# Optimization experiments

Measured on AMD Instinct MI355X. Metric: run time of the kernel, lower is better.

Reference implementation:

```python
import jax, jax.numpy as jnp
import numpy as np

G, N, F, D, L, H, MAXN, K = 256, 128, 128, 256, 4, 8, 512, 5
T = G * N
S = K + 1  # subgraph seq len: self + top-5 context nodes


def _ln(x, g, b, eps=1e-5):
    m = x.mean(-1, keepdims=True)
    v = ((x - m) ** 2).mean(-1, keepdims=True)
    return (x - m) / jnp.sqrt(v + eps) * g + b


def setup_inputs() -> dict:
    key = jax.random.key(0)
    ks = iter(jax.random.split(key, 40))
    r = lambda shape, s=0.02: jax.random.normal(next(ks), shape, jnp.float32) * s
    return {
        "x": jax.random.normal(next(ks), (T, F), jnp.float32),
        "W_raw": r((F, D)), "b_raw": jnp.zeros((D,), jnp.float32),
        "wl_emb": r((100, D)), "pos_emb": r((MAXN, D)), "hop_emb": r((MAXN, D)),
        "ln_g": jnp.ones((D,), jnp.float32), "ln_b": jnp.zeros((D,), jnp.float32),
        "Wqkv": r((L, D, 3 * D)), "bqkv": jnp.zeros((L, 3 * D), jnp.float32),
        "Wo": r((L, D, D)), "bo": jnp.zeros((L, D), jnp.float32),
        "n1_g": jnp.ones((L, D), jnp.float32), "n1_b": jnp.zeros((L, D), jnp.float32),
        "W1": r((L, D, 4 * D)), "b1": jnp.zeros((L, 4 * D), jnp.float32),
        "W2": r((L, 4 * D, D)), "b2": jnp.zeros((L, D), jnp.float32),
        "n2_g": jnp.ones((L, D), jnp.float32), "n2_b": jnp.zeros((L, D), jnp.float32),
        "W_res": r((F, D)), "b_res": jnp.zeros((D,), jnp.float32),
        "edge_index": jax.random.randint(next(ks), (2, 4 * T), 0, T, jnp.int32),
        "batch": jnp.repeat(jnp.arange(G, dtype=jnp.int32), N),
        "num_graphs": G,
    }


def _forward(x, W_raw, b_raw, wl_emb, pos_emb, hop_emb, ln_g, ln_b,
             Wqkv, bqkv, Wo, bo, n1_g, n1_b, W1, b1, W2, b2, n2_g, n2_b,
             W_res, b_res):
    # Inference path (training=False): intimacy matrix = eye(N) per graph, wl_codes = 0.
    eye = jnp.eye(N, dtype=x.dtype)
    _, topi = jax.lax.top_k(eye, K)                       # [N,K]: self first, then smallest tied-zero idxs
    idx = jnp.concatenate([jnp.arange(N)[:, None], topi], axis=1)  # [N,S] subgraph node ids (local)
    xg = x.reshape(G, N, F)
    sub_x = xg[:, idx]                                    # [G,N,S,F] gather per-node subgraphs
    raw = sub_x @ W_raw + b_raw                           # [G,N,S,D]
    dist = eye[jnp.arange(N)[:, None], idx]               # [N,S] intimacy of center to subgraph nodes
    hop_ids = jnp.where(dist > 0, (5.0 / jnp.maximum(dist, 1e-30)).astype(jnp.int32), MAXN - 1)
    hop_ids = jnp.clip(hop_ids, 0, MAXN - 1)              # [N,S]
    emb = raw + pos_emb[:S] + wl_emb[0] + hop_emb[hop_ids]
    h = _ln(emb, ln_g, ln_b).reshape(T, S, D)             # dropout is identity in eval
    # residual_mapped: only first num_graphs rows get non-zero residual (as in the source)
    res = jnp.zeros((T, S, D), x.dtype)
    res = res.at[:G].set((x @ W_res + b_res).reshape(G, N, D)[:, :S])
    hd = D // H
    scale = 1.0 / jnp.sqrt(jnp.asarray(hd, x.dtype))
    for l in range(L):
        qkv = h @ Wqkv[l] + bqkv[l]                       # [T,S,3D]
        q, k, v = jnp.split(qkv, 3, axis=-1)
        q = q.reshape(T, S, H, hd)
        k = k.reshape(T, S, H, hd)
        v = v.reshape(T, S, H, hd)
        sc = jnp.einsum('bqhd,bkhd->bhqk', q, k) * scale  # [T,H,S,S]
        a = jax.nn.softmax(sc, axis=-1)
        o = jnp.einsum('bhqk,bkhd->bqhd', a, v).reshape(T, S, D)
        attn = o @ Wo[l] + bo[l]
        h = _ln(h + attn + res, n1_g[l], n1_b[l])
        ff = jax.nn.gelu(h @ W1[l] + b1[l], approximate=False) @ W2[l] + b2[l]
        h = _ln(h + ff + res, n2_g[l], n2_b[l])
    return h[:, 0]                                        # [T,D] CLS/center-node output


def reference(x, W_raw, b_raw, wl_emb, pos_emb, hop_emb, ln_g, ln_b,
              Wqkv, bqkv, Wo, bo, n1_g, n1_b, W1, b1, W2, b2, n2_g, n2_b,
              W_res, b_res, edge_index, batch, num_graphs):
    # edge_index / batch / num_graphs are unused numerics in the eval path
    # (equal-size graphs assumed: batch = repeat(arange(G), N)).
    return _forward(x, W_raw, b_raw, wl_emb, pos_emb, hop_emb, ln_g, ln_b,
                    Wqkv, bqkv, Wo, bo, n1_g, n1_b, W1, b1, W2, b2, n2_g, n2_b,
                    W_res, b_res)
```

## Files before the change

### kernel.cpp

```cpp
#include <hip/hip_runtime.h>
#include <hip/hip_bf16.h>


#define TB 4
#define NROW 24

typedef float f32x4 __attribute__((ext_vector_type(4)));
typedef short bfv8  __attribute__((ext_vector_type(8)));

__device__ __forceinline__ float bf2f(__hip_bfloat16 v) { return __bfloat162float(v); }
__device__ __forceinline__ __hip_bfloat16 f2bf(float v) { return __float2bfloat16(v); }
__device__ __forceinline__ float bfs2f(short s) { return __uint_as_float(((unsigned)(unsigned short)s) << 16); }
__device__ __forceinline__ int swz(int row, int cb) { return row*512 + (cb ^ ((row & 7) << 4)); }
__device__ __forceinline__ float gelu_f(float v) { return 0.5f*v*(1.f + erff(v*0.70710678118654752f)); }
__device__ __forceinline__ float unpk(unsigned p, int hi) {
  return __uint_as_float(hi ? (p & 0xffff0000u) : (p << 16));
}

#define OWQ 0u
#define OWO 786432u
#define OW1 1048576u
#define OW2 2097152u
#define WS_ELEMS 3145728u
#define RESOFF    6291456u
#define ACTOFF    7864320u

__global__ __launch_bounds__(256) void gb_prep_kernel(
    const float* __restrict__ Wqkv, const float* __restrict__ Wo,
    const float* __restrict__ W1,   const float* __restrict__ W2,
    __hip_bfloat16* __restrict__ ws)
{
  int fg   = blockIdx.x * 4 + (threadIdx.x >> 6);
  int lane = threadIdx.x & 63;
  int layer = fg / 1536, r = fg % 1536;
  const float* src; int K, N, fl; unsigned dstbase;
  if (r < 384)       { src = Wqkv + layer*196608; K = 256;  N = 768;  fl = r;       dstbase = OWQ + layer*196608u; }
  else if (r < 512)  { src = Wo   + layer*65536;  K = 256;  N = 256;  fl = r - 384; dstbase = OWO + layer*65536u;  }
  else if (r < 1024) { src = W1   + layer*262144; K = 256;  N = 1024; fl = r - 512; dstbase = OW1 + layer*262144u; }
  else               { src = W2   + layer*262144; K = 1024; N = 256;  fl = r - 1024;dstbase = OW2 + layer*262144u; }
  int nk = K >> 5;
  int nt = fl / nk, ks = fl % nk;
  int n  = nt*16 + (lane & 15);
  int k0 = ks*32 + (lane >> 4)*8;
  __align__(16) __hip_bfloat16 tmp[8];
  #pragma unroll
  for (int j = 0; j < 8; ++j) tmp[j] = f2bf(src[(size_t)(k0 + j)*N + n]);
  *(uint4*)(ws + dstbase + (unsigned)fl*512u + lane*8) = *(const uint4*)tmp;
}

template<int NKTOT, class LoadA>
__device__ __forceinline__ void gemm_ks(const __hip_bfloat16* __restrict__ p,
                                        LoadA loadA, f32x4 (&C)[4][2])
{
  const unsigned ST = 4u*(unsigned)NKTOT*512u;
  bfv8 B[3][4];
  bfv8 a[2][4];
  #pragma unroll
  for (int i = 0; i < 4; ++i) {
    C[i][0] = (f32x4){0.f,0.f,0.f,0.f};
    C[i][1] = (f32x4){0.f,0.f,0.f,0.f};
  }
  #pragma unroll
  for (int k = 0; k < 4; ++k) B[0][k] = *(const bfv8*)(p + k*512);
  {
    const __hip_bfloat16* q = p + ST;
    #pragma unroll
    for (int k = 0; k < 4; ++k) B[1][k] = *(const bfv8*)(q + k*512);
  }
  loadA(0, a);
  #pragma unroll
  for (int s = 0; s < 8; ++s) {
    if (s + 2 < 8) {
      const __hip_bfloat16* q = p + (unsigned)((s+2) & 3)*ST + (unsigned)((s+2) >> 2)*2048u;
      #pragma unroll
      for (int k = 0; k < 4; ++k) B[(s+2)%3][k] = *(const bfv8*)(q + k*512);
    }
    if (s == 4) loadA(1, a);
    #pragma unroll
    for (int k = 0; k < 4; ++k) {
      C[s&3][0] = __builtin_amdgcn_mfma_f32_16x16x32_bf16(a[0][k], B[s%3][k], C[s&3][0], 0,0,0);
      C[s&3][1] = __builtin_amdgcn_mfma_f32_16x16x32_bf16(a[1][k], B[s%3][k], C[s&3][1], 0,0,0);
    }
  }
}

template<int NKTOT, class LoadA>
__device__ __forceinline__ void gemm_ksq(const __hip_bfloat16* __restrict__ p,
                                         LoadA loadA, f32x4 (&C)[2][2])
{
  const unsigned ST = 8u*(unsigned)NKTOT*512u;
  bfv8 a[2][2];
  #pragma unroll
  for (int i = 0; i < 2; ++i) {
    C[i][0] = (f32x4){0.f,0.f,0.f,0.f};
    C[i][1] = (f32x4){0.f,0.f,0.f,0.f};
  }
  #pragma unroll
  for (int q = 0; q < 4; ++q) {
    loadA(q, a);
    #pragma unroll
    for (int i = 0; i < 2; ++i) {
      const __hip_bfloat16* b = p + (unsigned)i*ST + (unsigned)q*1024u;
      bfv8 B0 = *(const bfv8*)(b);
      bfv8 B1 = *(const bfv8*)(b + 512);
      C[i][0] = __builtin_amdgcn_mfma_f32_16x16x32_bf16(a[0][0], B0, C[i][0], 0,0,0);
      C[i][1] = __builtin_amdgcn_mfma_f32_16x16x32_bf16(a[1][0], B0, C[i][1], 0,0,0);
      C[i][0] = __builtin_amdgcn_mfma_f32_16x16x32_bf16(a[0][1], B1, C[i][0], 0,0,0);
      C[i][1] = __builtin_amdgcn_mfma_f32_16x16x32_bf16(a[1][1], B1, C[i][1], 0,0,0);
    }
  }
}

template<int NKTOT, class LoadA>
__device__ __forceinline__ void gemm_ksq_acc(const __hip_bfloat16* __restrict__ p,
                                             LoadA loadA, f32x4 (&C)[2][2])
{
  const unsigned ST = 8u*(unsigned)NKTOT*512u;
  bfv8 a[2][2];
  #pragma unroll
  for (int q = 0; q < 4; ++q) {
    loadA(q, a);
    #pragma unroll
    for (int i = 0; i < 2; ++i) {
      const __hip_bfloat16* b = p + (unsigned)i*ST + (unsigned)q*1024u;
      bfv8 B0 = *(const bfv8*)(b);
      bfv8 B1 = *(const bfv8*)(b + 512);
      C[i][0] = __builtin_amdgcn_mfma_f32_16x16x32_bf16(a[0][0], B0, C[i][0], 0,0,0);
      C[i][1] = __builtin_amdgcn_mfma_f32_16x16x32_bf16(a[1][0], B0, C[i][1], 0,0,0);
      C[i][0] = __builtin_amdgcn_mfma_f32_16x16x32_bf16(a[0][1], B1, C[i][0], 0,0,0);
      C[i][1] = __builtin_amdgcn_mfma_f32_16x16x32_bf16(a[1][1], B1, C[i][1], 0,0,0);
    }
  }
}

__device__ __forceinline__ void ln24_norm(float* z, float* redbuf, float g, float b, int tid) {
  const int lane = tid & 63, wid = tid >> 6;
  float s1[NROW], s2[NROW];
  #pragma unroll
  for (int r = 0; r < NROW; ++r) { float v = z[r]; s1[r] = v; s2[r] = v*v; }
  #pragma unroll
  for (int off = 32; off; off >>= 1) {
    #pragma unroll
    for (int r = 0; r < NROW; ++r) {
      s1[r] += __shfl_down(s1[r], off, 64);
      s2[r] += __shfl_down(s2[r], off, 64);
    }
  }
  if (lane == 0) {
    #pragma unroll
    for (int r = 0; r < NROW; ++r) { redbuf[wid*48 + r] = s1[r]; redbuf[wid*48 + 24 + r] = s2[r]; }
  }
  __syncthreads();
  #pragma unroll
  for (int r = 0; r < NROW; ++r) {
    float S1 = redbuf[r] + redbuf[48+r] + redbuf[96+r] + redbuf[144+r];
    float S2 = redbuf[24+r] + redbuf[72+r] + redbuf[120+r] + redbuf[168+r];
    float m  = S1 * (1.0f/256.0f);
    float var = S2 * (1.0f/256.0f) - m*m;
    float iv = rsqrtf(var + 1e-5f);
    z[r] = (z[r] - m) * iv * g + b;
  }
  __syncthreads();
}


__global__ __launch_bounds__(256) void mk_embed(
    const float* __restrict__ x,
    const float* __restrict__ W_raw, const float* __restrict__ b_raw,
    const float* __restrict__ wl_emb, const float* __restrict__ pos_emb,
    const float* __restrict__ hop_emb,
    const float* __restrict__ ln_g, const float* __restrict__ ln_b,
    const float* __restrict__ W_res, const float* __restrict__ b_res,
    __hip_bfloat16* __restrict__ h0, float* __restrict__ res, int t0)
{
  __shared__ float xbuf[24][128];
  __shared__ float zb[24][256];
  __shared__ float part[2][24][8];
  __shared__ float stat[24][2];
  const int tid = threadIdx.x;
  const int bt  = blockIdx.x;

  for (int idx = tid; idx < 24*128; idx += 256) {
    int tt = idx / 768, rem = idx % 768;
    int s = rem >> 7, f = rem & 127;
    int t = t0 + bt*4 + tt, g = t >> 7, i = t & 127;
    int node;
    if (s < 2) node = i;
    else { int j = s - 2; node = (j < i) ? j : (j + 1); }
    xbuf[tt*6+s][f] = x[(g*128 + node)*128 + f];
  }
  __syncthreads();

  {
    float z[NROW];
    #pragma unroll
    for (int r = 0; r < NROW; ++r) z[r] = 0.f;
    #pragma unroll 2
    for (int f4 = 0; f4 < 32; ++f4) {
      float w0 = W_raw[(f4*4+0)*256 + tid];
      float w1 = W_raw[(f4*4+1)*256 + tid];
      float w2 = W_raw[(f4*4+2)*256 + tid];
      float w3 = W_raw[(f4*4+3)*256 + tid];
      #pragma unroll
      for (int r = 0; r < NROW; ++r) {
        float4 xv = *(const float4*)(&xbuf[r][f4*4]);
        z[r] += xv.x*w0 + xv.y*w1 + xv.z*w2 + xv.w*w3;
      }
    }
    float br  = b_raw[tid];
    float wl  = wl_emb[tid];
    float hp0 = hop_emb[5*256 + tid];
    float hp1 = hop_emb[511*256 + tid];
    float p[6];
    #pragma unroll
    for (int s = 0; s < 6; ++s) p[s] = pos_emb[s*256 + tid];
    #pragma unroll
    for (int r = 0; r < NROW; ++r) {
      int s = r % 6;
      zb[r][tid] = z[r] + br + p[s] + wl + ((s < 2) ? hp0 : hp1);
    }
  }
  __syncthreads();

  if (tid < 192) {
    int row = tid >> 3, seg = tid & 7;
    float s1 = 0.f, s2 = 0.f;
    #pragma unroll
    for (int i = 0; i < 32; ++i) {
      int col = seg*32 + ((i + tid) & 31);
      float v = zb[row][col];
      s1 += v; s2 += v*v;
    }
    part[0][row][seg] = s1; part[1][row][seg] = s2;
  }
  __syncthreads();
  if (tid < 24) {
    float S1 = 0.f, S2 = 0.f;
    #pragma unroll
    for (int k = 0; k < 8; ++k) { S1 += part[0][tid][k]; S2 += part[1][tid][k]; }
    float m = S1 * (1.0f/256.0f);
    float var = S2 * (1.0f/256.0f) - m*m;
    stat[tid][0] = m; stat[tid][1] = rsqrtf(var + 1e-5f);
  }
  __syncthreads();
  {
    float g = ln_g[tid], b = ln_b[tid];
    #pragma unroll
    for (int r = 0; r < NROW; ++r) {
      float v = (zb[r][tid] - stat[r][0]) * stat[r][1] * g + b;
      h0[(size_t)(bt*24 + r)*256 + tid] = f2bf(v);
    }
  }

  if (t0 + bt*4 < 256) {
    __syncthreads();
    for (int idx = tid; idx < 24*128; idx += 256) {
      int tt = idx / 768, rem = idx % 768;
      int s = rem >> 7, f = rem & 127;
      int t = t0 + bt*4 + tt;
      xbuf[tt*6+s][f] = x[(t*128 + s)*128 + f];
    }
    __syncthreads();
    float resv[NROW];
    float brr = b_res[tid];
    #pragma unroll
    for (int r = 0; r < NROW; ++r) resv[r] = brr;
    #pragma unroll 2
    for (int f4 = 0; f4 < 32; ++f4) {
      float w0 = W_res[(f4*4+0)*256 + tid];
      float w1 = W_res[(f4*4+1)*256 + tid];
      float w2 = W_res[(f4*4+2)*256 + tid];
      float w3 = W_res[(f4*4+3)*256 + tid];
      #pragma unroll
      for (int r = 0; r < NROW; ++r) {
        float4 xv = *(const float4*)(&xbuf[r][f4*4]);
        resv[r] += xv.x*w0 + xv.y*w1 + xv.z*w2 + xv.w*w3;
      }
    }
    #pragma unroll
    for (int r = 0; r < NROW; ++r)
      res[(size_t)((t0 + bt*4)*6 + r)*256 + tid] = resv[r];
  }
}

__device__ __forceinline__ void stageA(const __hip_bfloat16* __restrict__ src,
                                       int row0, int stride, char* aT, int tid) {
  #pragma unroll
  for (int k = 0; k < 4; ++k) {
    int cid = tid + k*256;
    int row = cid >> 5, cc = cid & 31;
    uint4 v = *(const uint4*)(src + (size_t)(row0 + row)*stride + cc*8);
    *(uint4*)(aT + swz(row, cc*16)) = v;
  }
}
__device__ __forceinline__ void stageA512(const __hip_bfloat16* __restrict__ src,
                                          int row0, int stride, char* aT, int tid) {
  #pragma unroll
  for (int k = 0; k < 2; ++k) {
    int cid = tid + k*512;
    int row = cid >> 5, cc = cid & 31;
    uint4 v = *(const uint4*)(src + (size_t)(row0 + row)*stride + cc*8);
    *(uint4*)(aT + swz(row, cc*16)) = v;
  }
}

__global__ __launch_bounds__(256) void mk_qkv(
    const __hip_bfloat16* __restrict__ h, const __hip_bfloat16* __restrict__ Wf,
    const float* __restrict__ bqkv_l, __hip_bfloat16* __restrict__ qkv)
{
  __shared__ __align__(16) char aT[16384];
  const int tid = threadIdx.x;
  const int lane = tid & 63, wid = tid >> 6;
  const int l15 = lane & 15, l4 = lane >> 4;
  const int row0 = blockIdx.x * 32;

  stageA(h, row0, 256, aT, tid);
  __syncthreads();

  auto lA = [&](int kh, bfv8 (&a)[2][4]) {
    #pragma unroll
    for (int k = 0; k < 4; ++k) {
      a[0][k] = *(const bfv8*)(aT + swz(l15,      (kh*4 + k)*64 + l4*16));
      a[1][k] = *(const bfv8*)(aT + swz(16 + l15, (kh*4 + k)*64 + l4*16));
    }
  };

  #pragma unroll 1
  for (int sub = 0; sub < 3; ++sub) {
    f32x4 C[4][2];
    gemm_ks<8>(Wf + (unsigned)(sub*16 + wid)*8u*512u + lane*8, lA, C);
    #pragma unroll
    for (int i = 0; i < 4; ++i) {
      int col = sub*256 + (wid + i*4)*16 + l15;
      float bb = bqkv_l[col];
      #pragma unroll
      for (int j = 0; j < 4; ++j) {
        qkv[(size_t)(row0 + l4*4 + j)*768 + col]      = f2bf(C[i][0][j] + bb);
        qkv[(size_t)(row0 + 16 + l4*4 + j)*768 + col] = f2bf(C[i][1][j] + bb);
      }
    }
  }
}

__global__ __launch_bounds__(256) void mk_attn(__hip_bfloat16* __restrict__ qkv)
{
  const int tid = threadIdx.x;
  const int tl = tid >> 3, hh = tid & 7;
  const size_t rowbase = (size_t)(blockIdx.x*32 + tl)*6;
  const int cb = hh*32;

  #pragma unroll 1
  for (int q = 0; q < 6; ++q) {
    const __hip_bfloat16* qr = qkv + (rowbase + q)*768 + cb;
    bfv8 qv[4];
    #pragma unroll
    for (int p4 = 0; p4 < 4; ++p4) qv[p4] = *(const bfv8*)(qr + p4*8);
    float a[6]; float mx = -1e30f;
    #pragma unroll
    for (int sp = 0; sp < 6; ++sp) {
      const __hip_bfloat16* kr = qkv + (rowbase + sp)*768 + 256 + cb;
      float s = 0.f;
      #pragma unroll
      for (int p4 = 0; p4 < 4; ++p4) {
        bfv8 kv = *(const bfv8*)(kr + p4*8);
        #pragma unroll
        for (int j = 0; j < 8; ++j) s += bfs2f(qv[p4][j]) * bfs2f(kv[j]);
      }
      a[sp] = s * 0.17677669529663687f;
      mx = fmaxf(mx, a[sp]);
    }
    float sum = 0.f;
    #pragma unroll
    for (int sp = 0; sp < 6; ++sp) { a[sp] = __expf(a[sp] - mx); sum += a[sp]; }
    float inv = 1.f / sum;
    #pragma unroll
    for (int sp = 0; sp < 6; ++sp) a[sp] *= inv;
    float oc[32];
    #pragma unroll
    for (int j = 0; j < 32; ++j) oc[j] = 0.f;
    #pragma unroll
    for (int sp = 0; sp < 6; ++sp) {
      const __hip_bfloat16* vr = qkv + (rowbase + sp)*768 + 512 + cb;
      float asp = a[sp];
      #pragma unroll
      for (int p4 = 0; p4 < 4; ++p4) {
        bfv8 vv = *(const bfv8*)(vr + p4*8);
        #pragma unroll
        for (int j = 0; j < 8; ++j) oc[p4*8 + j] += asp * bfs2f(vv[j]);
      }
    }
    __hip_bfloat16* orow = qkv + (rowbase + q)*768 + cb;
    #pragma unroll
    for (int p4 = 0; p4 < 4; ++p4) {
      __align__(16) __hip_bfloat16 ob[8];
      #pragma unroll
      for (int j = 0; j < 8; ++j) ob[j] = f2bf(oc[p4*8 + j]);
      *(uint4*)(orow + p4*8) = *(const uint4*)ob;
    }
  }
}

__global__ __launch_bounds__(512) void mk_wo_ln(
    const __hip_bfloat16* __restrict__ qkv ,
    const __hip_bfloat16* __restrict__ h,
    const float* __restrict__ res,
    const __hip_bfloat16* __restrict__ Wf, const float* __restrict__ bo_l,
    const float* __restrict__ gln, const float* __restrict__ bln,
    __hip_bfloat16* __restrict__ h1, int t0)
{
  __shared__ __align__(16) char smem[37120];
  char* aT = smem;
  float (*zb)[256]      = (float (*)[256])smem;
  float (*part)[32][16] = (float (*)[32][16])(smem + 32768);
  float (*stat)[2]      = (float (*)[2])(smem + 32768 + 4096);
  const int tid = threadIdx.x;
  const int lane = tid & 63, wid = tid >> 6;
  const int l15 = lane & 15, l4 = lane >> 4;
  const int row0 = blockIdx.x * 32;

  stageA512(qkv, row0, 768, aT, tid);
  __syncthreads();

  auto lAq = [&](int q, bfv8 (&a)[2][2]) {
    #pragma unroll
    for (int k = 0; k < 2; ++k) {
      a[0][k] = *(const bfv8*)(aT + swz(l15,      (q*2 + k)*64 + l4*16));
      a[1][k] = *(const bfv8*)(aT + swz(16 + l15, (q*2 + k)*64 + l4*16));
    }
  };

  {
    f32x4 C[2][2];
    gemm_ksq<8>(Wf + (unsigned)wid*8u*512u + lane*8, lAq, C);
    __syncthreads();
    #pragma unroll
    for (int i = 0; i < 2; ++i) {
      int col = (wid + i*8)*16 + l15;
      #pragma unroll
      for (int j = 0; j < 4; ++j) {
        zb[l4*4 + j][col]      = C[i][0][j];
        zb[16 + l4*4 + j][col] = C[i][1][j];
      }
    }
  }
  __syncthreads();

  #pragma unroll 4
  for (int it = 0; it < 16; ++it) {
    int idx = tid + it*512, row = idx >> 8, col = idx & 255;
    float v = zb[row][col] + bf2f(h[(size_t)(row0 + row)*256 + col]) + bo_l[col];
    int grow = t0*6 + row0 + row;
    if (grow < 1536) v += res[(size_t)grow*256 + col];
    zb[row][col] = v;
  }
  __syncthreads();

  {
    int row = tid >> 4, seg = tid & 15;
    float s1 = 0.f, s2 = 0.f;
    #pragma unroll
    for (int i = 0; i < 16; ++i) {
      int col = seg*16 + ((i + tid) & 15);
      float v = zb[row][col];
      s1 += v; s2 += v*v;
    }
    part[0][row][seg] = s1; part[1][row][seg] = s2;
  }
  __syncthreads();
  if (tid < 32) {
    float S1 = 0.f, S2 = 0.f;
    #pragma unroll
    for (int k = 0; k < 16; ++k) { S1 += part[0][tid][k]; S2 += part[1][tid][k]; }
    float m = S1 * (1.0f/256.0f);
    float var = S2 * (1.0f/256.0f) - m*m;
    stat[tid][0] = m; stat[tid][1] = rsqrtf(var + 1e-5f);
  }
  __syncthreads();
  #pragma unroll 4
  for (int it = 0; it < 16; ++it) {
    int idx = tid + it*512, row = idx >> 8, col = idx & 255;
    float v = (zb[row][col] - stat[row][0]) * stat[row][1] * gln[col] + bln[col];
    h1[(size_t)(row0 + row)*256 + col] = f2bf(v);
  }
}

__global__ __launch_bounds__(512) void mk_ffn(
    const __hip_bfloat16* __restrict__ h1,
    const __hip_bfloat16* __restrict__ W1f, const __hip_bfloat16* __restrict__ W2f,
    const float* __restrict__ b1_l, const float* __restrict__ b2_l,
    const float* __restrict__ gln, const float* __restrict__ bln,
    const float* __restrict__ res, __hip_bfloat16* __restrict__ hout,
    float* __restrict__ outp, int t0)
{
  __shared__ __align__(16) char smem[37120];
  char* aT = smem;
  char* gT = smem + 16384;
  float (*zf)[256]      = (float (*)[256])smem;
  float (*part)[32][16] = (float (*)[32][16])(smem + 32768);
  float (*stat)[2]      = (float (*)[2])(smem + 32768 + 4096);
  const int tid = threadIdx.x;
  const int lane = tid & 63, wid = tid >> 6;
  const int l15 = lane & 15, l4 = lane >> 4;
  const int row0 = blockIdx.x * 32;

  stageA512(h1, row0, 256, aT, tid);
  __syncthreads();

  auto lAq = [&](int q, bfv8 (&a)[2][2]) {
    #pragma unroll
    for (int k = 0; k < 2; ++k) {
      a[0][k] = *(const bfv8*)(aT + swz(l15,      (q*2 + k)*64 + l4*16));
      a[1][k] = *(const bfv8*)(aT + swz(16 + l15, (q*2 + k)*64 + l4*16));
    }
  };
  auto lGq = [&](int q, bfv8 (&a)[2][2]) {
    #pragma unroll
    for (int k = 0; k < 2; ++k) {
      a[0][k] = *(const bfv8*)(gT + swz(l15,      (q*2 + k)*64 + l4*16));
      a[1][k] = *(const bfv8*)(gT + swz(16 + l15, (q*2 + k)*64 + l4*16));
    }
  };

  f32x4 Cff[2][2];
  #pragma unroll
  for (int i = 0; i < 2; ++i) {
    Cff[i][0] = (f32x4){0.f,0.f,0.f,0.f};
    Cff[i][1] = (f32x4){0.f,0.f,0.f,0.f};
  }

  #pragma unroll 1
  for (int ch = 0; ch < 4; ++ch) {
    {
      f32x4 C[2][2];
      gemm_ksq<8>(W1f + (unsigned)(ch*16 + wid)*8u*512u + lane*8, lAq, C);
      #pragma unroll
      for (int i = 0; i < 2; ++i) {
        int colR = (wid + i*8)*16 + l15;
        float bb = b1_l[ch*256 + colR];
        int col2 = colR*2;
        #pragma unroll
        for (int j = 0; j < 4; ++j) {
          *(__hip_bfloat16*)(gT + swz(l4*4 + j, col2))      = f2bf(gelu_f(C[i][0][j] + bb));
          *(__hip_bfloat16*)(gT + swz(16 + l4*4 + j, col2)) = f2bf(gelu_f(C[i][1][j] + bb));
        }
      }
    }
    __syncthreads();
    gemm_ksq_acc<32>(W2f + (unsigned)(wid*32 + ch*8)*512u + lane*8, lGq, Cff);
    __syncthreads();
  }

  #pragma unroll
  for (int i = 0; i < 2; ++i) {
    int col = (wid + i*8)*16 + l15;
    float b2v = b2_l[col];
    #pragma unroll
    for (int j = 0; j < 4; ++j) {
      int r0 = l4*4 + j, r1 = 16 + l4*4 + j;
      float v0 = Cff[i][0][j] + bf2f(h1[(size_t)(row0 + r0)*256 + col]) + b2v;
      float v1 = Cff[i][1][j] + bf2f(h1[(size_t)(row0 + r1)*256 + col]) + b2v;
      int g0 = t0*6 + row0 + r0, g1 = t0*6 + row0 + r1;
      if (g0 < 1536) v0 += res[(size_t)g0*256 + col];
      if (g1 < 1536) v1 += res[(size_t)g1*256 + col];
      zf[r0][col] = v0;
      zf[r1][col] = v1;
    }
  }
  __syncthreads();
  {
    int row = tid >> 4, seg = tid & 15;
    float s1 = 0.f, s2 = 0.f;
    #pragma unroll
    for (int i = 0; i < 16; ++i) {
      int col = seg*16 + ((i + tid) & 15);
      float v = zf[row][col];
      s1 += v; s2 += v*v;
    }
    part[0][row][seg] = s1; part[1][row][seg] = s2;
  }
  __syncthreads();
  if (tid < 32) {
    float S1 = 0.f, S2 = 0.f;
    #pragma unroll
    for (int k = 0; k < 16; ++k) { S1 += part[0][tid][k]; S2 += part[1][tid][k]; }
    float m = S1 * (1.0f/256.0f);
    float var = S2 * (1.0f/256.0f) - m*m;
    stat[tid][0] = m; stat[tid][1] = rsqrtf(var + 1e-5f);
  }
  __syncthreads();
  #pragma unroll 4
  for (int it = 0; it < 16; ++it) {
    int idx = tid + it*512, row = idx >> 8, col = idx & 255;
    float v = (zf[row][col] - stat[row][0]) * stat[row][1] * gln[col] + bln[col];
    hout[(size_t)(row0 + row)*256 + col] = f2bf(v);
    if (outp && ((row0 + row) % 6 == 0)) {
      int gtok = t0 + (row0 + row) / 6;
      outp[(size_t)gtok*256 + col] = v;
    }
  }
}

__global__ __launch_bounds__(256, 2) void gb_mfma_kernel(
    const float* __restrict__ x,
    const float* __restrict__ W_raw, const float* __restrict__ b_raw,
    const float* __restrict__ wl_emb, const float* __restrict__ pos_emb,
    const float* __restrict__ hop_emb,
    const float* __restrict__ ln_g, const float* __restrict__ ln_b,
    const float* __restrict__ bqkv, const float* __restrict__ bo,
    const float* __restrict__ n1g,  const float* __restrict__ n1b,
    const float* __restrict__ b1,   const float* __restrict__ b2,
    const float* __restrict__ n2g,  const float* __restrict__ n2b,
    const float* __restrict__ W_res, const float* __restrict__ b_res,
    const __hip_bfloat16* __restrict__ wf,
    float* __restrict__ out)
{
  __shared__ __align__(16) char smem[75392];
  char* hsb = smem;
  char* uA  = smem + 16384;
  char* uB  = smem + 53632;
  float (*attw)[24][6] = (float (*)[24][6])(smem + 70016);
  float* redbuf = (float*)(smem + 74624);

  __hip_bfloat16 (*qkvs)[776] = (__hip_bfloat16 (*)[776])uA;
  float (*fbuf)[264] = (float (*)[264])uA;
  float (*xbuf)[128] = (float (*)[128])uA;

  const int tid  = threadIdx.x;
  const int bt   = blockIdx.x;
  const int lane = tid & 63, wid = tid >> 6;
  const int l15  = lane & 15, l4 = lane >> 4;

  auto mkA = [l15, l4](const char* buf) {
    return [buf, l15, l4](int kh, bfv8 (&a)[2][4]) {
      #pragma unroll
      for (int k = 0; k < 4; ++k) {
        a[0][k] = *(const bfv8*)(buf + swz(l15,      (kh*4 + k)*64 + l4*16));
        a[1][k] = *(const bfv8*)(buf + swz(16 + l15, (kh*4 + k)*64 + l4*16));
      }
    };
  };

  {
    uint4 zz = {0u,0u,0u,0u};
    *(uint4*)(hsb + 24*512 + tid*16) = zz;
    *(uint4*)(uB  + 24*512 + tid*16) = zz;
  }

  for (int idx = tid; idx < TB*6*128; idx += 256) {
    int tt = idx / 768, rem = idx % 768;
    int s = rem >> 7, f = rem & 127;
    int t = bt*TB + tt, g = t >> 7, i = t & 127;
    int node;
    if (s < 2) node = i;
    else { int j = s - 2; node = (j < i) ? j : (j + 1); }
    xbuf[tt*6+s][f] = x[(g*128 + node)*128 + f];
  }
  __syncthreads();

  {
    float z[NROW];
    #pragma unroll
    for (int r = 0; r < NROW; ++r) z[r] = 0.f;
    #pragma unroll 2
    for (int f4 = 0; f4 < 32; ++f4) {
      float w0 = W_raw[(f4*4+0)*256 + tid];
      float w1 = W_raw[(f4*4+1)*256 + tid];
      float w2 = W_raw[(f4*4+2)*256 + tid];
      float w3 = W_raw[(f4*4+3)*256 + tid];
      #pragma unroll
      for (int r = 0; r < NROW; ++r) {
        float4 xv = *(const float4*)(&xbuf[r][f4*4]);
        z[r] += xv.x*w0 + xv.y*w1 + xv.z*w2 + xv.w*w3;
      }
    }
    float br  = b_raw[tid];
    float wl  = wl_emb[tid];
    float hp0 = hop_emb[5*256 + tid];
    float hp1 = hop_emb[511*256 + tid];
    float p[6];
    #pragma unroll
    for (int s = 0; s < 6; ++s) p[s] = pos_emb[s*256 + tid];
    #pragma unroll
    for (int r = 0; r < NROW; ++r) {
      int s = r % 6;
      z[r] += br + p[s] + wl + ((s < 2) ? hp0 : hp1);
    }
    ln24_norm(z, redbuf, ln_g[tid], ln_b[tid], tid);
    #pragma unroll
    for (int r = 0; r < NROW; ++r)
      *(__hip_bfloat16*)(hsb + swz(r, tid*2)) = f2bf(z[r]);
  }

  unsigned resp[12];
  #pragma unroll
  for (int k = 0; k < 12; ++k) resp[k] = 0u;
  if (bt < 64) {
    __syncthreads();
    for (int idx = tid; idx < TB*6*128; idx += 256) {
      int tt = idx / 768, rem = idx % 768;
      int s = rem >> 7, f = rem & 127;
      int t = bt*TB + tt;
      xbuf[tt*6+s][f] = x[(t*128 + s)*128 + f];
    }
    __syncthreads();
    float resv[NROW];
    float brr = b_res[tid];
    #pragma unroll
    for (int r = 0; r < NROW; ++r) resv[r] = brr;
    #pragma unroll 2
    for (int f4 = 0; f4 < 32; ++f4) {
      float w0 = W_res[(f4*4+0)*256 + tid];
      float w1 = W_res[(f4*4+1)*256 + tid];
      float w2 = W_res[(f4*4+2)*256 + tid];
      float w3 = W_res[(f4*4+3)*256 + tid];
      #pragma unroll
      for (int r = 0; r < NROW; ++r) {
        float4 xv = *(const float4*)(&xbuf[r][f4*4]);
        resv[r] += xv.x*w0 + xv.y*w1 + xv.z*w2 + xv.w*w3;
      }
    }
    #pragma unroll
    for (int k = 0; k < 12; ++k) {
      unsigned lo = __float_as_uint(resv[2*k])   >> 16;
      unsigned hi = __float_as_uint(resv[2*k+1]) & 0xffff0000u;
      resp[k] = hi | lo;
    }
  }

  float z[NROW];

  #pragma unroll 1
  for (int l = 0; l < 4; ++l) {
    const __hip_bfloat16* WQf = wf + OWQ + (unsigned)l*196608u;
    const __hip_bfloat16* WOf = wf + OWO + (unsigned)l*65536u;
    const __hip_bfloat16* W1f = wf + OW1 + (unsigned)l*262144u;
    const __hip_bfloat16* W2f = wf + OW2 + (unsigned)l*262144u;

    __syncthreads();

    {
      auto lA = mkA(hsb);
      #pragma unroll 1
      for (int sub = 0; sub < 3; ++sub) {
        f32x4 C[4][2];
        gemm_ks<8>(WQf + (unsigned)(sub*16 + wid)*8u*512u + lane*8, lA, C);
        #pragma unroll
        for (int i = 0; i < 4; ++i) {
          int gcol = sub*256 + (wid + i*4)*16 + l15;
          float bbv = bqkv[l*768 + gcol];
          #pragma unroll
          for (int j = 0; j < 4; ++j) {
            qkvs[l4*4 + j][gcol] = f2bf(C[i][0][j] + bbv);
            int r1 = 16 + l4*4 + j;
            if (r1 < NROW) qkvs[r1][gcol] = f2bf(C[i][1][j] + bbv);
          }
        }
      }
    }
    __syncthreads();

    if (tid < 192) {
      int hh = tid / 24, r = tid % 24;
      int tt6 = (r / 6) * 6;
      bfv8 qv[4];
      #pragma unroll
      for (int p4 = 0; p4 < 4; ++p4) qv[p4] = *(const bfv8*)(&qkvs[r][hh*32 + p4*8]);
      float sc[6];
      #pragma unroll
      for (int sp = 0; sp < 6; ++sp) {
        float s = 0.f;
        #pragma unroll
        for (int p4 = 0; p4 < 4; ++p4) {
          bfv8 kv = *(const bfv8*)(&qkvs[tt6 + sp][256 + hh*32 + p4*8]);
          #pragma unroll
          for (int j = 0; j < 8; ++j) s += bfs2f(qv[p4][j]) * bfs2f(kv[j]);
        }
        sc[sp] = s * 0.17677669529663687f;
      }
      float mx = sc[0];
      #pragma unroll
      for (int sp = 1; sp < 6; ++sp) mx = fmaxf(mx, sc[sp]);
      float sum = 0.f;
      #pragma unroll
      for (int sp = 0; sp < 6; ++sp) { sc[sp] = __expf(sc[sp] - mx); sum += sc[sp]; }
      float inv = 1.f / sum;
      #pragma unroll
      for (int sp = 0; sp < 6; ++sp) attw[hh][r][sp] = sc[sp] * inv;
    }
    __syncthreads();

    {
      int hh = tid >> 5, c = tid & 31;
      int col2 = (hh*32 + c)*2;
      #pragma unroll
      for (int tt = 0; tt < 4; ++tt) {
        float vv[6];
        #pragma unroll
        for (int sp = 0; sp < 6; ++sp) vv[sp] = bf2f(qkvs[tt*6 + sp][512 + hh*32 + c]);
        #pragma unroll
        for (int q = 0; q < 6; ++q) {
          float o = 0.f;
          #pragma unroll
          for (int sp = 0; sp < 6; ++sp) o += attw[hh][tt*6 + q][sp] * vv[sp];
          *(__hip_bfloat16*)(uB + swz(tt*6 + q, col2)) = f2bf(o);
        }
      }
    }
    __syncthreads();

    {
      f32x4 C[4][2];
      gemm_ks<8>(WOf + (unsigned)wid*8u*512u + lane*8, mkA(uB), C);
      #pragma unroll
      for (int i = 0; i < 4; ++i) {
        int col = (wid + i*4)*16 + l15;
        #pragma unroll
        for (int j = 0; j < 4; ++j) {
          fbuf[l4*4 + j][col] = C[i][0][j];
          int r1 = 16 + l4*4 + j;
          if (r1 < NROW) fbuf[r1][col] = C[i][1][j];
        }
      }
    }
    __syncthreads();

    {
      float bov = bo[l*256 + tid];
      #pragma unroll
      for (int r = 0; r < NROW; ++r)
        z[r] = bf2f(*(const __hip_bfloat16*)(hsb + swz(r, tid*2)))
             + unpk(resp[r >> 1], r & 1) + fbuf[r][tid] + bov;
    }
    #pragma unroll
    for (int k = 0; k < 12; ++k) *(unsigned*)(uB + (k*256 + tid)*4) = 0u;
    ln24_norm(z, redbuf, n1g[l*256 + tid], n1b[l*256 + tid], tid);
    #pragma unroll
    for (int r = 0; r < NROW; ++r)
      *(__hip_bfloat16*)(hsb + swz(r, tid*2)) = f2bf(z[r]);
    {
      uint4 zz = {0u,0u,0u,0u};
      *(uint4*)(uA + 24*512 + tid*16) = zz;
      *(uint4*)(uA + 16384 + 24*512 + tid*16) = zz;
    }
    __syncthreads();

    {
      auto lAh = mkA(hsb);
      #pragma unroll 1
      for (int ch = 0; ch < 4; ++ch) {
        char* gb = uA + (ch & 1)*16384;
        {
          f32x4 C[4][2];
          gemm_ks<8>(W1f + (unsigned)(ch*128 + wid*8)*512u + lane*8, lAh, C);
          #pragma unroll
          for (int i = 0; i < 4; ++i) {
            float bbv = b1[l*1024 + ch*256 + (wid + i*4)*16 + l15];
            int col2 = ((wid + i*4)*16 + l15)*2;
            #pragma unroll
            for (int j = 0; j < 4; ++j) {
              *(__hip_bfloat16*)(gb + swz(l4*4 + j, col2)) = f2bf(gelu_f(C[i][0][j] + bbv));
              int r1 = 16 + l4*4 + j;
              if (r1 < NROW)
                *(__hip_bfloat16*)(gb + swz(r1, col2)) = f2bf(gelu_f(C[i][1][j] + bbv));
            }
          }
        }
        __syncthreads();
        {
          f32x4 C[4][2];
          gemm_ks<32>(W2f + (unsigned)(wid*32 + ch*8)*512u + lane*8, mkA(gb), C);
          #pragma unroll
          for (int i = 0; i < 4; ++i) {
            int col2 = ((wid + i*4)*16 + l15)*2;
            #pragma unroll
            for (int j = 0; j < 4; ++j) {
              {
                __hip_bfloat16* pp = (__hip_bfloat16*)(uB + (l4*4 + j)*512 + col2);
                *pp = f2bf(bf2f(*pp) + C[i][0][j]);
              }
              int r1 = 16 + l4*4 + j;
              if (r1 < NROW) {
                __hip_bfloat16* pp = (__hip_bfloat16*)(uB + r1*512 + col2);
                *pp = f2bf(bf2f(*pp) + C[i][1][j]);
              }
            }
          }
        }
      }
    }
    __syncthreads();

    {
      float b2v = b2[l*256 + tid];
      #pragma unroll
      for (int r = 0; r < NROW; ++r)
        z[r] = bf2f(*(const __hip_bfloat16*)(hsb + swz(r, tid*2)))
             + unpk(resp[r >> 1], r & 1)
             + bf2f(*(const __hip_bfloat16*)(uB + r*512 + tid*2)) + b2v;
    }
    ln24_norm(z, redbuf, n2g[l*256 + tid], n2b[l*256 + tid], tid);
    #pragma unroll
    for (int r = 0; r < NROW; ++r)
      *(__hip_bfloat16*)(hsb + swz(r, tid*2)) = f2bf(z[r]);
  }

  #pragma unroll
  for (int tt = 0; tt < TB; ++tt)
    out[(bt*TB + tt)*256 + tid] = z[tt*6];
}

__global__ __launch_bounds__(256, 2) void gb_fused_fallback(
    const float* __restrict__ x,
    const float* __restrict__ W_raw, const float* __restrict__ b_raw,
    const float* __restrict__ wl_emb, const float* __restrict__ pos_emb,
    const float* __restrict__ hop_emb,
    const float* __restrict__ ln_g, const float* __restrict__ ln_b,
    const float* __restrict__ Wqkv, const float* __restrict__ bqkv,
    const float* __restrict__ Wo,   const float* __restrict__ bo,
    const float* __restrict__ n1g,  const float* __restrict__ n1b,
    const float* __restrict__ W1,   const float* __restrict__ b1,
    const float* __restrict__ W2,   const float* __restrict__ b2,
    const float* __restrict__ n2g,  const float* __restrict__ n2b,
    const float* __restrict__ W_res, const float* __restrict__ b_res,
    float* __restrict__ out)
{
  __shared__ float hs[NROW][256];
  __shared__ __align__(16) char bufraw[NROW*768*2];
  __shared__ float attw[8][NROW][8];
  __shared__ float redbuf[192];

  __hip_bfloat16 (*qkvs)[768] = (__hip_bfloat16 (*)[768])bufraw;
  float (*fbuf)[256] = (float (*)[256])bufraw;
  float (*xbuf)[128] = (float (*)[128])bufraw;

  const int tid = threadIdx.x;
  const int bt  = blockIdx.x;

  for (int idx = tid; idx < TB*6*128; idx += 256) {
    int tt = idx / 768, rem = idx % 768;
    int s = rem >> 7, f = rem & 127;
    int t = bt*TB + tt, g = t >> 7, i = t & 127;
    int node;
    if (s < 2) node = i;
    else { int j = s - 2; node = (j < i) ? j : (j + 1); }
    xbuf[tt*6+s][f] = x[(g*128 + node)*128 + f];
  }
  __syncthreads();

  float z[NROW];
  {
    #pragma unroll
    for (int r = 0; r < NROW; ++r) z[r] = 0.f;
    #pragma unroll 4
    for (int f = 0; f < 128; ++f) {
      float w = W_raw[f*256 + tid];
      #pragma unroll
      for (int r = 0; r < NROW; ++r) z[r] += xbuf[r][f] * w;
    }
    float br  = b_raw[tid];
    float wl  = wl_emb[tid];
    float hp0 = hop_emb[5*256 + tid];
    float hp1 = hop_emb[511*256 + tid];
    float p[6];
    #pragma unroll
    for (int s = 0; s < 6; ++s) p[s] = pos_emb[s*256 + tid];
    #pragma unroll
    for (int r = 0; r < NROW; ++r) {
      int s = r % 6;
      z[r] += br + p[s] + wl + ((s < 2) ? hp0 : hp1);
    }
  }
  ln24_norm(z, redbuf, ln_g[tid], ln_b[tid], tid);
  #pragma unroll
  for (int r = 0; r < NROW; ++r) hs[r][tid] = z[r];

  float resv[NROW];
  #pragma unroll
  for (int r = 0; r < NROW; ++r) resv[r] = 0.f;
  if (bt < 64) {
    __syncthreads();
    for (int idx = tid; idx < TB*6*128; idx += 256) {
      int tt = idx / 768, rem = idx % 768;
      int s = rem >> 7, f = rem & 127;
      int t = bt*TB + tt;
      xbuf[tt*6+s][f] = x[(t*128 + s)*128 + f];
    }
    __syncthreads();
    #pragma unroll 4
    for (int f = 0; f < 128; ++f) {
      float w = W_res[f*256 + tid];
      #pragma unroll
      for (int r = 0; r < NROW; ++r) resv[r] += xbuf[r][f] * w;
    }
    float brr = b_res[tid];
    #pragma unroll
    for (int r = 0; r < NROW; ++r) resv[r] += brr;
  }

  for (int l = 0; l < 4; ++l) {
    const float* Wqkv_l = Wqkv + l*196608;
    const float* bqkv_l = bqkv + l*768;
    const float* Wo_l   = Wo   + l*65536;
    const float* bo_l   = bo   + l*256;
    const float* W1_l   = W1   + l*262144;
    const float* b1_l   = b1   + l*1024;
    const float* W2_l   = W2   + l*262144;
    const float* b2_l   = b2   + l*256;

    __syncthreads();

    for (int cg = 0; cg < 3; ++cg) {
      int col = cg*256 + tid;
      float acc[NROW];
      #pragma unroll
      for (int r = 0; r < NROW; ++r) acc[r] = 0.f;
      #pragma unroll 4
      for (int kk = 0; kk < 256; ++kk) {
        float w = Wqkv_l[kk*768 + col];
        #pragma unroll
        for (int r = 0; r < NROW; ++r) acc[r] += hs[r][kk] * w;
      }
      float bbv = bqkv_l[col];
      #pragma unroll
      for (int r = 0; r < NROW; ++r) qkvs[r][col] = f2bf(acc[r] + bbv);
    }
    __syncthreads();

    #pragma unroll 1
    for (int it = 0; it < 5; ++it) {
      int idx = it*256 + tid;
      if (idx < 1152) {
        int hh = idx / 144, rem = idx % 144;
        int r = rem / 6, sp = rem % 6;
        int tt6 = (r / 6) * 6;
        float sc = 0.f;
        #pragma unroll
        for (int c = 0; c < 32; ++c)
          sc += bf2f(qkvs[r][hh*32 + c]) * bf2f(qkvs[tt6 + sp][256 + hh*32 + c]);
        attw[hh][r][sp] = sc * 0.17677669529663687f;
      }
    }
    __syncthreads();

    if (tid < 192) {
      int hh = tid / 24, r = tid % 24;
      float mx = attw[hh][r][0];
      #pragma unroll
      for (int sp = 1; sp < 6; ++sp) mx = fmaxf(mx, attw[hh][r][sp]);
      float e[6], sum = 0.f;
      #pragma unroll
      for (int sp = 0; sp < 6; ++sp) { e[sp] = expf(attw[hh][r][sp] - mx); sum += e[sp]; }
      float inv = 1.f / sum;
      #pragma unroll
      for (int sp = 0; sp < 6; ++sp) attw[hh][r][sp] = e[sp] * inv;
    }
    __syncthreads();

    float oreg[NROW];
    {
      int hh = tid >> 5, c = tid & 31;
      #pragma unroll
      for (int r = 0; r < NROW; ++r) {
        int tt6 = (r / 6) * 6;
        float o = 0.f;
        #pragma unroll
        for (int sp = 0; sp < 6; ++sp)
          o += attw[hh][r][sp] * bf2f(qkvs[tt6 + sp][512 + hh*32 + c]);
        oreg[r] = o;
      }
    }
    __syncthreads();
    #pragma unroll
    for (int r = 0; r < NROW; ++r) fbuf[r][tid] = oreg[r];
    __syncthreads();

    {
      float bod = bo_l[tid];
      float zz[NROW];
      #pragma unroll
      for (int r = 0; r < NROW; ++r) zz[r] = bod;
      #pragma unroll 4
      for (int kk = 0; kk < 256; ++kk) {
        float w = Wo_l[kk*256 + tid];
        #pragma unroll
        for (int r = 0; r < NROW; ++r) zz[r] += fbuf[r][kk] * w;
      }
      #pragma unroll
      for (int r = 0; r < NROW; ++r) z[r] += zz[r] + resv[r];
    }
    ln24_norm(z, redbuf, n1g[l*256 + tid], n1b[l*256 + tid], tid);
    #pragma unroll
    for (int r = 0; r < NROW; ++r) hs[r][tid] = z[r];
    __syncthreads();

    float ffv[NROW];
    {
      float b2d = b2_l[tid];
      #pragma unroll
      for (int r = 0; r < NROW; ++r) ffv[r] = b2d;
    }
    for (int ch = 0; ch < 4; ++ch) {
      int j = ch*256 + tid;
      float gvv[NROW];
      float b1j = b1_l[j];
      #pragma unroll
      for (int r = 0; r < NROW; ++r) gvv[r] = b1j;
      #pragma unroll 4
      for (int kk = 0; kk < 256; ++kk) {
        float w = W1_l[kk*1024 + j];
        #pragma unroll
        for (int r = 0; r < NROW; ++r) gvv[r] += hs[r][kk] * w;
      }
      __syncthreads();
      #pragma unroll
      for (int r = 0; r < NROW; ++r) fbuf[r][tid] = gelu_f(gvv[r]);
      __syncthreads();
      #pragma unroll 4
      for (int kk = 0; kk < 256; ++kk) {
        float w = W2_l[(ch*256 + kk)*256 + tid];
        #pragma unroll
        for (int r = 0; r < NROW; ++r) ffv[r] += fbuf[r][kk] * w;
      }
    }
    #pragma unroll
    for (int r = 0; r < NROW; ++r) z[r] += ffv[r] + resv[r];
    ln24_norm(z, redbuf, n2g[l*256 + tid], n2b[l*256 + tid], tid);
    #pragma unroll
    for (int r = 0; r < NROW; ++r) hs[r][tid] = z[r];
  }

  __syncthreads();
  #pragma unroll
  for (int tt = 0; tt < TB; ++tt)
    out[(bt*TB + tt)*256 + tid] = hs[tt*6][tid];
}

extern "C" void kernel_launch(void* const* d_in, const int* in_sizes, int n_in,
                              void* d_out, int out_size, void* d_ws, size_t ws_size,
                              hipStream_t stream) {
  (void)in_sizes; (void)n_in; (void)out_size;
  const float* x      = (const float*)d_in[0];
  const float* W_raw  = (const float*)d_in[1];
  const float* b_raw  = (const float*)d_in[2];
  const float* wl_emb = (const float*)d_in[3];
  const float* pos_emb= (const float*)d_in[4];
  const float* hop_emb= (const float*)d_in[5];
  const float* ln_g   = (const float*)d_in[6];
  const float* ln_b   = (const float*)d_in[7];
  const float* Wqkv   = (const float*)d_in[8];
  const float* bqkv   = (const float*)d_in[9];
  const float* Wo     = (const float*)d_in[10];
  const float* bo     = (const float*)d_in[11];
  const float* n1g    = (const float*)d_in[12];
  const float* n1b    = (const float*)d_in[13];
  const float* W1     = (const float*)d_in[14];
  const float* b1     = (const float*)d_in[15];
  const float* W2     = (const float*)d_in[16];
  const float* b2     = (const float*)d_in[17];
  const float* n2g    = (const float*)d_in[18];
  const float* n2b    = (const float*)d_in[19];
  const float* W_res  = (const float*)d_in[20];
  const float* b_res  = (const float*)d_in[21];

  int tc = 0;
  for (int cand = 32768; cand >= 4096; cand >>= 1) {
    size_t need = (size_t)ACTOFF + (size_t)cand * 15360u;
    if (ws_size >= need) { tc = cand; break; }
  }

  if (tc > 0) {
    char* wsb = (char*)d_ws;
    __hip_bfloat16* wf  = (__hip_bfloat16*)wsb;
    float*          res = (float*)(wsb + RESOFF);
    __hip_bfloat16* h0  = (__hip_bfloat16*)(wsb + ACTOFF);
    __hip_bfloat16* h1  = (__hip_bfloat16*)(wsb + ACTOFF + (size_t)tc*6*512);
    __hip_bfloat16* qkv = (__hip_bfloat16*)(wsb + ACTOFF + (size_t)tc*6*1024);
    float* outp = (float*)d_out;

    gb_prep_kernel<<<1536, 256, 0, stream>>>(Wqkv, Wo, W1, W2, wf);

    int nchunk = 32768 / tc;
    for (int c = 0; c < nchunk; ++c) {
      int t0 = c * tc;
      mk_embed<<<tc/4, 256, 0, stream>>>(x, W_raw, b_raw, wl_emb, pos_emb,
          hop_emb, ln_g, ln_b, W_res, b_res, h0, res, t0);
      for (int l = 0; l < 4; ++l) {
        mk_qkv<<<tc*6/32, 256, 0, stream>>>(
            h0, wf + OWQ + (unsigned)l*196608u, bqkv + l*768, qkv);
        mk_attn<<<tc/32, 256, 0, stream>>>(qkv);
        mk_wo_ln<<<tc*6/32, 512, 0, stream>>>(
            qkv, h0, res, wf + OWO + (unsigned)l*65536u, bo + l*256,
            n1g + l*256, n1b + l*256, h1, t0);
        mk_ffn<<<tc*6/32, 512, 0, stream>>>(
            h1, wf + OW1 + (unsigned)l*262144u, wf + OW2 + (unsigned)l*262144u,
            b1 + l*1024, b2 + l*256, n2g + l*256, n2b + l*256,
            res, h0, (l == 3) ? outp : (float*)nullptr, t0);
      }
    }
  } else if (ws_size >= (size_t)WS_ELEMS * 2) {
    __hip_bfloat16* wsb = (__hip_bfloat16*)d_ws;
    gb_prep_kernel<<<1536, 256, 0, stream>>>(Wqkv, Wo, W1, W2, wsb);
    gb_mfma_kernel<<<8192, 256, 0, stream>>>(
        x, W_raw, b_raw, wl_emb, pos_emb, hop_emb, ln_g, ln_b,
        bqkv, bo, n1g, n1b, b1, b2, n2g, n2b, W_res, b_res,
        wsb, (float*)d_out);
  } else {
    gb_fused_fallback<<<8192, 256, 0, stream>>>(
        x, W_raw, b_raw, wl_emb, pos_emb, hop_emb, ln_g, ln_b,
        Wqkv, bqkv, Wo, bo, n1g, n1b, W1, b1, W2, b2, n2g, n2b,
        W_res, b_res, (float*)d_out);
  }
}
```

Measured before the change: 3.003 ms.

## Compute x@W_raw once per node and gather projected rows in embed

The embedding projection x@W_raw is now computed once per node in a separate kernel, instead of once per subgraph slot (six rows per node). The embed kernel gathers the precomputed projected rows by node index, which cuts the embedding GEMM FLOPs by about six times. The cost is an extra kernel launch and a round-trip of fp32 intermediates through the h1 workspace buffer. The gather also relies on every neighbor node lying inside the current chunk, which holds because chunks are aligned to whole graphs.

After: 2.788 ms. 1.08x faster.

```diff
diff --git a/kernel.cpp b/kernel.cpp
--- a/kernel.cpp
+++ b/kernel.cpp
@@ -164,9 +164,44 @@
 }
 
 
-__global__ __launch_bounds__(256) void mk_embed(
-    const float* __restrict__ x,
-    const float* __restrict__ W_raw, const float* __restrict__ b_raw,
+__global__ __launch_bounds__(256) void mk_xw(
+    const float* __restrict__ x, const float* __restrict__ W_raw,
+    float* __restrict__ y, int t0)
+{
+  __shared__ float xbuf[16][128];
+  const int tid = threadIdx.x;
+  const int row0 = t0 + blockIdx.x * 16;
+
+  #pragma unroll
+  for (int k = 0; k < 8; ++k) {
+    int idx = tid + k*256;
+    xbuf[idx >> 7][idx & 127] = x[(size_t)(row0 + (idx >> 7))*128 + (idx & 127)];
+  }
+  __syncthreads();
+
+  float z[16];
+  #pragma unroll
+  for (int r = 0; r < 16; ++r) z[r] = 0.f;
+  #pragma unroll 2
+  for (int f4 = 0; f4 < 32; ++f4) {
+    float w0 = W_raw[(f4*4+0)*256 + tid];
+    float w1 = W_raw[(f4*4+1)*256 + tid];
+    float w2 = W_raw[(f4*4+2)*256 + tid];
+    float w3 = W_raw[(f4*4+3)*256 + tid];
+    #pragma unroll
+    for (int r = 0; r < 16; ++r) {
+      float4 xv = *(const float4*)(&xbuf[r][f4*4]);
+      z[r] += xv.x*w0 + xv.y*w1 + xv.z*w2 + xv.w*w3;
+    }
+  }
+  #pragma unroll
+  for (int r = 0; r < 16; ++r)
+    y[(size_t)(blockIdx.x*16 + r)*256 + tid] = z[r];
+}
+
+__global__ __launch_bounds__(256) void mk_embed2(
+    const float* __restrict__ x, const float* __restrict__ y,
+    const float* __restrict__ b_raw,
     const float* __restrict__ wl_emb, const float* __restrict__ pos_emb,
     const float* __restrict__ hop_emb,
     const float* __restrict__ ln_g, const float* __restrict__ ln_b,
@@ -180,33 +215,7 @@
   const int tid = threadIdx.x;
   const int bt  = blockIdx.x;
 
-  for (int idx = tid; idx < 24*128; idx += 256) {
-    int tt = idx / 768, rem = idx % 768;
-    int s = rem >> 7, f = rem & 127;
-    int t = t0 + bt*4 + tt, g = t >> 7, i = t & 127;
-    int node;
-    if (s < 2) node = i;
-    else { int j = s - 2; node = (j < i) ? j : (j + 1); }
-    xbuf[tt*6+s][f] = x[(g*128 + node)*128 + f];
-  }
-  __syncthreads();
-
   {
-    float z[NROW];
-    #pragma unroll
-    for (int r = 0; r < NROW; ++r) z[r] = 0.f;
-    #pragma unroll 2
-    for (int f4 = 0; f4 < 32; ++f4) {
-      float w0 = W_raw[(f4*4+0)*256 + tid];
-      float w1 = W_raw[(f4*4+1)*256 + tid];
-      float w2 = W_raw[(f4*4+2)*256 + tid];
-      float w3 = W_raw[(f4*4+3)*256 + tid];
-      #pragma unroll
-      for (int r = 0; r < NROW; ++r) {
-        float4 xv = *(const float4*)(&xbuf[r][f4*4]);
-        z[r] += xv.x*w0 + xv.y*w1 + xv.z*w2 + xv.w*w3;
-      }
-    }
     float br  = b_raw[tid];
     float wl  = wl_emb[tid];
     float hp0 = hop_emb[5*256 + tid];
@@ -216,8 +225,13 @@
     for (int s = 0; s < 6; ++s) p[s] = pos_emb[s*256 + tid];
     #pragma unroll
     for (int r = 0; r < NROW; ++r) {
-      int s = r % 6;
-      zb[r][tid] = z[r] + br + p[s] + wl + ((s < 2) ? hp0 : hp1);
+      int t = t0 + bt*4 + (r / 6), s = r % 6;
+      int g = t >> 7, i = t & 127;
+      int node;
+      if (s < 2) node = i;
+      else { int j = s - 2; node = (j < i) ? j : (j + 1); }
+      float yv = y[(size_t)(g*128 + node - t0)*256 + tid];
+      zb[r][tid] = yv + br + p[s] + wl + ((s < 2) ? hp0 : hp1);
     }
   }
   __syncthreads();
@@ -1175,6 +1189,7 @@
     __hip_bfloat16* h0  = (__hip_bfloat16*)(wsb + ACTOFF);
     __hip_bfloat16* h1  = (__hip_bfloat16*)(wsb + ACTOFF + (size_t)tc*6*512);
     __hip_bfloat16* qkv = (__hip_bfloat16*)(wsb + ACTOFF + (size_t)tc*6*1024);
+    float* y = (float*)h1;
     float* outp = (float*)d_out;
 
     gb_prep_kernel<<<1536, 256, 0, stream>>>(Wqkv, Wo, W1, W2, wf);
@@ -1182,7 +1197,8 @@
     int nchunk = 32768 / tc;
     for (int c = 0; c < nchunk; ++c) {
       int t0 = c * tc;
-      mk_embed<<<tc/4, 256, 0, stream>>>(x, W_raw, b_raw, wl_emb, pos_emb,
+      mk_xw<<<tc/16, 256, 0, stream>>>(x, W_raw, y, t0);
+      mk_embed2<<<tc/4, 256, 0, stream>>>(x, y, b_raw, wl_emb, pos_emb,
           hop_emb, ln_g, ln_b, W_res, b_res, h0, res, t0);
       for (int l = 0; l < 4; ++l) {
         mk_qkv<<<tc*6/32, 256, 0, stream>>>(
```
